# Optimization experiments

Measured on AMD Instinct MI355X. Metric: run time of the kernel, lower is better.

The kernel has to match this reference:

```python
import jax, jax.numpy as jnp
import numpy as np

N_NODES = 50000
N_EDGES = 640000
DIM_IN = 128
DIM_OUT = 128
NUM_GRAPHS = 64


def setup_inputs() -> dict:
    key = jax.random.key(0)
    ks = jax.random.split(key, 8)
    x = jax.random.normal(ks[0], (N_NODES, DIM_IN), dtype=jnp.float32)
    edge_index = jax.random.randint(ks[1], (2, N_EDGES), 0, N_NODES, dtype=jnp.int32)
    batch = jnp.sort(jax.random.randint(ks[2], (N_NODES,), 0, NUM_GRAPHS, dtype=jnp.int32))
    s = 1.0 / np.sqrt(DIM_IN)
    W1 = jax.random.normal(ks[3], (DIM_IN, DIM_IN), dtype=jnp.float32) * s
    W2 = jax.random.normal(ks[4], (DIM_IN, DIM_IN), dtype=jnp.float32) * s
    Wlin = jax.random.normal(ks[5], (DIM_IN, DIM_OUT), dtype=jnp.float32) * s
    b1 = jnp.zeros((DIM_IN,), jnp.float32)
    b2 = jnp.zeros((DIM_IN,), jnp.float32)
    blin = jnp.zeros((DIM_OUT,), jnp.float32)
    return {"x": x, "edge_index": edge_index, "batch": batch,
            "W1": W1, "b1": b1, "W2": W2, "b2": b2, "Wlin": Wlin, "blin": blin}


def _gcn_conv(x, W, b, src, dst, n_nodes):
    # GCNConv: symmetric norm with self-loops: D^{-1/2}(A+I)D^{-1/2} X W + b
    h = x @ W                                                   # [N, d]
    deg = jax.ops.segment_sum(jnp.ones_like(dst, jnp.float32), dst,
                              num_segments=n_nodes) + 1.0       # +1 self loop
    dinv = jax.lax.rsqrt(deg)                                   # [N]
    w = dinv[src] * dinv[dst]                                   # per-edge norm [E]
    agg = jax.ops.segment_sum(h[src] * w[:, None], dst, num_segments=n_nodes)
    return agg + h * (dinv * dinv)[:, None] + b                 # self-loop term + bias


def reference(x, edge_index, batch, W1, b1, W2, b2, Wlin, blin):
    n = x.shape[0]
    src, dst = edge_index[0], edge_index[1]
    h = jax.nn.relu(_gcn_conv(x, W1, b1, src, dst, n))          # dropout = identity (eval)
    h = _gcn_conv(h, W2, b2, src, dst, n)
    # global mean pool over graphs
    s = jax.ops.segment_sum(h, batch, num_segments=NUM_GRAPHS)  # [G, d]
    cnt = jax.ops.segment_sum(jnp.ones((n,), jnp.float32), batch, num_segments=NUM_GRAPHS)
    pooled = s / jnp.maximum(cnt, 1.0)[:, None]
    return jax.nn.relu(pooled @ Wlin + blin)
```

## Files before the change

### kernel.cpp

```cpp
#include <hip/hip_runtime.h>

#define N_NODES   50000
#define N_EDGES   640000
#define DIM       128
#define NUM_GRAPHS 64
#define SLOTS     64
#define FILL_BLOCKS  1250
#define GEMM1_BLOCKS 196

typedef __attribute__((ext_vector_type(8))) short          s16x8;
typedef __attribute__((ext_vector_type(8))) unsigned short u16x8;
typedef __attribute__((ext_vector_type(4))) float          f32x4;

__device__ inline float bf2f(unsigned short u) {
    unsigned v = ((unsigned)u) << 16;
    float f;
    __builtin_memcpy(&f, &v, 4);
    return f;
}
__device__ inline unsigned short f2bf(float f) {
    unsigned u;
    __builtin_memcpy(&u, &f, 4);
    u = (u + 0x7fffu + ((u >> 16) & 1u)) >> 16;
    return (unsigned short)u;
}

__global__ __launch_bounds__(128) void k_prep_w(const float* __restrict__ W1,
                                                const float* __restrict__ W2,
                                                unsigned short* __restrict__ Wt1,
                                                unsigned short* __restrict__ Wt2,
                                                int* __restrict__ cnt,
                                                float* __restrict__ pooled) {
    int k = blockIdx.x & 127;
    const float*    W  = (blockIdx.x < DIM) ? W1 : W2;
    unsigned short* Wt = (blockIdx.x < DIM) ? Wt1 : Wt2;
    int n = threadIdx.x;
    Wt[n * DIM + k] = f2bf(W[k * DIM + n]);

    int gid = blockIdx.x * 128 + threadIdx.x;
    for (int i = gid; i < N_NODES; i += 32768) cnt[i] = 0;
    if (gid < NUM_GRAPHS * DIM) pooled[gid] = 0.f;
}

__global__ __launch_bounds__(512) void k_fill_gemm1(const int* __restrict__ src,
                                                    const int* __restrict__ dst,
                                                    int* __restrict__ cnt,
                                                    unsigned short* __restrict__ slots,
                                                    const float* __restrict__ x,
                                                    const unsigned short* __restrict__ Wt1,
                                                    unsigned short* __restrict__ H1) {
    __shared__ unsigned short wsh[DIM][136];
    const int tid = threadIdx.x;

    if (blockIdx.x < FILL_BLOCKS) {
        int e = blockIdx.x * 512 + tid;
        int s = src[e], d = dst[e];
        int p = atomicAdd(&cnt[d], 1);
        if (p < SLOTS) slots[d * SLOTS + p] = (unsigned short)s;
        return;
    }

    const int gb = blockIdx.x - FILL_BLOCKS;

    #pragma unroll
    for (int i = 0; i < 4; i++) {
        int off = tid * 8 + i * 4096;
        int r = off >> 7, cc = off & 127;
        u16x8 v = *reinterpret_cast<const u16x8*>(Wt1 + off);
        *reinterpret_cast<u16x8*>(&wsh[r][cc]) = v;
    }
    __syncthreads();

    const int wid  = tid >> 6;
    const int lane = tid & 63;
    const int l15  = lane & 15;
    const int lk   = lane >> 4;
    const int row0 = gb * 256 + wid * 32;

    f32x4 acc[2][8];
    #pragma unroll
    for (int a = 0; a < 2; a++)
        #pragma unroll
        for (int n = 0; n < 8; n++) acc[a][n] = (f32x4){0.f, 0.f, 0.f, 0.f};

    const long long r0 = min(row0 + l15,      N_NODES - 1);
    const long long r1 = min(row0 + 16 + l15, N_NODES - 1);

    #pragma unroll
    for (int kk = 0; kk < 4; kk++) {
        const int kb = kk * 32 + lk * 8;
        s16x8 a0, a1;
        const float4 p0 = *reinterpret_cast<const float4*>(x + r0 * DIM + kb);
        const float4 q0 = *reinterpret_cast<const float4*>(x + r0 * DIM + kb + 4);
        const float4 p1 = *reinterpret_cast<const float4*>(x + r1 * DIM + kb);
        const float4 q1 = *reinterpret_cast<const float4*>(x + r1 * DIM + kb + 4);
        a0[0]=(short)f2bf(p0.x); a0[1]=(short)f2bf(p0.y); a0[2]=(short)f2bf(p0.z); a0[3]=(short)f2bf(p0.w);
        a0[4]=(short)f2bf(q0.x); a0[5]=(short)f2bf(q0.y); a0[6]=(short)f2bf(q0.z); a0[7]=(short)f2bf(q0.w);
        a1[0]=(short)f2bf(p1.x); a1[1]=(short)f2bf(p1.y); a1[2]=(short)f2bf(p1.z); a1[3]=(short)f2bf(p1.w);
        a1[4]=(short)f2bf(q1.x); a1[5]=(short)f2bf(q1.y); a1[6]=(short)f2bf(q1.z); a1[7]=(short)f2bf(q1.w);
        #pragma unroll
        for (int n = 0; n < 8; n++) {
            s16x8 b = *reinterpret_cast<const s16x8*>(&wsh[n * 16 + l15][kb]);
            acc[0][n] = __builtin_amdgcn_mfma_f32_16x16x32_bf16(a0, b, acc[0][n], 0, 0, 0);
            acc[1][n] = __builtin_amdgcn_mfma_f32_16x16x32_bf16(a1, b, acc[1][n], 0, 0, 0);
        }
    }

    #pragma unroll
    for (int rh = 0; rh < 2; rh++) {
        #pragma unroll
        for (int j = 0; j < 4; j++) {
            int row = row0 + rh * 16 + lk * 4 + j;
            if (row < N_NODES) {
                #pragma unroll
                for (int n = 0; n < 8; n++)
                    H1[(long long)row * DIM + n * 16 + l15] = f2bf(acc[rh][n][j]);
            }
        }
    }
}

__global__ __launch_bounds__(512) void k_gemm2(const unsigned short* __restrict__ Ab,
                                               const unsigned short* __restrict__ Wt,
                                               unsigned short* __restrict__ H) {
    __shared__ unsigned short wsh[DIM][136];
    const int tid = threadIdx.x;

    #pragma unroll
    for (int i = 0; i < 4; i++) {
        int off = tid * 8 + i * 4096;
        int r = off >> 7, cc = off & 127;
        u16x8 v = *reinterpret_cast<const u16x8*>(Wt + off);
        *reinterpret_cast<u16x8*>(&wsh[r][cc]) = v;
    }
    __syncthreads();

    const int wid  = tid >> 6;
    const int lane = tid & 63;
    const int l15  = lane & 15;
    const int lk   = lane >> 4;
    const int row0 = blockIdx.x * 256 + wid * 32;

    f32x4 acc[2][8];
    #pragma unroll
    for (int a = 0; a < 2; a++)
        #pragma unroll
        for (int n = 0; n < 8; n++) acc[a][n] = (f32x4){0.f, 0.f, 0.f, 0.f};

    const long long r0 = min(row0 + l15,      N_NODES - 1);
    const long long r1 = min(row0 + 16 + l15, N_NODES - 1);

    #pragma unroll
    for (int kk = 0; kk < 4; kk++) {
        const int kb = kk * 32 + lk * 8;
        s16x8 a0 = *reinterpret_cast<const s16x8*>(Ab + r0 * DIM + kb);
        s16x8 a1 = *reinterpret_cast<const s16x8*>(Ab + r1 * DIM + kb);
        #pragma unroll
        for (int n = 0; n < 8; n++) {
            s16x8 b = *reinterpret_cast<const s16x8*>(&wsh[n * 16 + l15][kb]);
            acc[0][n] = __builtin_amdgcn_mfma_f32_16x16x32_bf16(a0, b, acc[0][n], 0, 0, 0);
            acc[1][n] = __builtin_amdgcn_mfma_f32_16x16x32_bf16(a1, b, acc[1][n], 0, 0, 0);
        }
    }

    #pragma unroll
    for (int rh = 0; rh < 2; rh++) {
        #pragma unroll
        for (int j = 0; j < 4; j++) {
            int row = row0 + rh * 16 + lk * 4 + j;
            if (row < N_NODES) {
                #pragma unroll
                for (int n = 0; n < 8; n++)
                    H[(long long)row * DIM + n * 16 + l15] = f2bf(acc[rh][n][j]);
            }
        }
    }
}

__device__ inline void gather_node(const int* __restrict__ cnt,
                                   const unsigned short* __restrict__ slots,
                                   const unsigned short* __restrict__ h,
                                   const float* __restrict__ bias,
                                   int n, int c, float dn, float* acc) {
    float d2 = dn * dn;
    u16x8 hv = *reinterpret_cast<const u16x8*>(h + (size_t)n * DIM + c);
    #pragma unroll
    for (int j = 0; j < 8; j++) acc[j] = bf2f(hv[j]) * d2 + bias[c + j];

    const int m = min(cnt[n], SLOTS);
    const unsigned short* sl = slots + (size_t)n * SLOTS;

    int i = 0;
    for (; i + 3 < m; i += 4) {
        int s0 = sl[i], s1 = sl[i + 1], s2 = sl[i + 2], s3 = sl[i + 3];
        float w0 = rsqrtf((float)cnt[s0] + 1.0f) * dn;
        float w1 = rsqrtf((float)cnt[s1] + 1.0f) * dn;
        float w2 = rsqrtf((float)cnt[s2] + 1.0f) * dn;
        float w3 = rsqrtf((float)cnt[s3] + 1.0f) * dn;
        u16x8 v0 = *reinterpret_cast<const u16x8*>(h + (size_t)s0 * DIM + c);
        u16x8 v1 = *reinterpret_cast<const u16x8*>(h + (size_t)s1 * DIM + c);
        u16x8 v2 = *reinterpret_cast<const u16x8*>(h + (size_t)s2 * DIM + c);
        u16x8 v3 = *reinterpret_cast<const u16x8*>(h + (size_t)s3 * DIM + c);
        #pragma unroll
        for (int j = 0; j < 8; j++)
            acc[j] += (bf2f(v0[j]) * w0 + bf2f(v1[j]) * w1) +
                      (bf2f(v2[j]) * w2 + bf2f(v3[j]) * w3);
    }
    for (; i < m; i++) {
        int s0 = sl[i];
        float w0 = rsqrtf((float)cnt[s0] + 1.0f) * dn;
        u16x8 v0 = *reinterpret_cast<const u16x8*>(h + (size_t)s0 * DIM + c);
        #pragma unroll
        for (int j = 0; j < 8; j++) acc[j] += bf2f(v0[j]) * w0;
    }
}

__global__ __launch_bounds__(256) void k_pull1(const int* __restrict__ cnt,
                                               const unsigned short* __restrict__ slots,
                                               const unsigned short* __restrict__ h,
                                               const float* __restrict__ bias,
                                               unsigned short* __restrict__ outp) {
    int gid = blockIdx.x * blockDim.x + threadIdx.x;
    int n = gid >> 4;
    if (n >= N_NODES) return;
    int c = (gid & 15) << 3;

    float dn = rsqrtf((float)cnt[n] + 1.0f);
    float acc[8];
    gather_node(cnt, slots, h, bias, n, c, dn, acc);

    u16x8 o;
    #pragma unroll
    for (int j = 0; j < 8; j++) o[j] = f2bf(fmaxf(acc[j], 0.f));
    *reinterpret_cast<u16x8*>(outp + (size_t)n * DIM + c) = o;
}

__global__ __launch_bounds__(256) void k_pull_pool(const int* __restrict__ cnt,
                                                   const unsigned short* __restrict__ slots,
                                                   const unsigned short* __restrict__ h,
                                                   const float* __restrict__ bias,
                                                   const int* __restrict__ batch,
                                                   float* __restrict__ pooled) {
    __shared__ float pool_l[2][DIM];
    const int tid  = threadIdx.x;
    const int base = blockIdx.x * 64;
    const int c    = (tid & 15) << 3;

    pool_l[tid >> 7][tid & 127] = 0.f;
    __syncthreads();

    const int gmin = batch[min(base, N_NODES - 1)];

    #pragma unroll
    for (int r = 0; r < 4; r++) {
        int n = base + r * 16 + (tid >> 4);
        bool valid = n < N_NODES;
        int nn = min(n, N_NODES - 1);

        float dn = rsqrtf((float)cnt[nn] + 1.0f);
        float acc[8];
        gather_node(cnt, slots, h, bias, nn, c, dn, acc);
        if (!valid) {
            #pragma unroll
            for (int j = 0; j < 8; j++) acc[j] = 0.f;
        }

        const int g = batch[nn];
        const int d = g - gmin;

        if (__all(g == __shfl(g, 0))) {
            #pragma unroll
            for (int j = 0; j < 8; j++) {
                acc[j] += __shfl_xor(acc[j], 16);
                acc[j] += __shfl_xor(acc[j], 32);
            }
            if ((tid & 63) < 16) {
                if (d < 2) {
                    #pragma unroll
                    for (int j = 0; j < 8; j++) atomicAdd(&pool_l[d][c + j], acc[j]);
                } else {
                    #pragma unroll
                    for (int j = 0; j < 8; j++) atomicAdd(&pooled[g * DIM + c + j], acc[j]);
                }
            }
        } else {
            if (d < 2) {
                #pragma unroll
                for (int j = 0; j < 8; j++) atomicAdd(&pool_l[d][c + j], acc[j]);
            } else {
                #pragma unroll
                for (int j = 0; j < 8; j++) atomicAdd(&pooled[g * DIM + c + j], acc[j]);
            }
        }
    }
    __syncthreads();

    const int f = tid & 127;
    if (tid < 128) {
        atomicAdd(&pooled[gmin * DIM + f], pool_l[0][f]);
    } else {
        int last = min(base + 63, N_NODES - 1);
        if (batch[last] > gmin) atomicAdd(&pooled[(gmin + 1) * DIM + f], pool_l[1][f]);
    }
}

__global__ __launch_bounds__(128) void k_pool2(const float* __restrict__ pooled,
                                               const int* __restrict__ batch,
                                               const float* __restrict__ Wlin,
                                               const float* __restrict__ blin,
                                               float* __restrict__ out) {
    int g = blockIdx.x;
    int t = threadIdx.x;
    __shared__ int se[2];
    __shared__ float pr[DIM];
    if (t < 2) {
        int target = g + t;
        int lo = 0, hi = N_NODES;
        while (lo < hi) { int mid = (lo + hi) >> 1; if (batch[mid] < target) lo = mid + 1; else hi = mid; }
        se[t] = lo;
    }
    __syncthreads();
    float inv_cnt = 1.0f / fmaxf((float)(se[1] - se[0]), 1.0f);
    pr[t] = pooled[g * DIM + t] * inv_cnt;
    __syncthreads();
    float acc = blin[t];
    #pragma unroll 8
    for (int k = 0; k < DIM; k++) acc += pr[k] * Wlin[k * DIM + t];
    out[g * DIM + t] = fmaxf(acc, 0.f);
}

extern "C" void kernel_launch(void* const* d_in, const int* in_sizes, int n_in,
                              void* d_out, int out_size, void* d_ws, size_t ws_size,
                              hipStream_t stream) {
    const float* x          = (const float*)d_in[0];
    const int*   edge_index = (const int*)d_in[1];
    const int*   batch      = (const int*)d_in[2];
    const float* W1         = (const float*)d_in[3];
    const float* b1         = (const float*)d_in[4];
    const float* W2         = (const float*)d_in[5];
    const float* b2         = (const float*)d_in[6];
    const float* Wlin       = (const float*)d_in[7];
    const float* blin       = (const float*)d_in[8];
    float*       out        = (float*)d_out;

    const int* src = edge_index;
    const int* dst = edge_index + N_EDGES;

    char* ws = (char*)d_ws;
    size_t off = 0;
    auto alloc = [&](size_t bytes) { void* p = ws + off; off = (off + bytes + 255) & ~255ULL; return p; };
    int*            cnt    = (int*)            alloc((size_t)N_NODES * 4);
    unsigned short* slots  = (unsigned short*) alloc((size_t)N_NODES * SLOTS * 2);
    float*          pooled = (float*)          alloc((size_t)NUM_GRAPHS * DIM * 4);
    unsigned short* Wt1    = (unsigned short*) alloc((size_t)DIM * DIM * 2);
    unsigned short* Wt2    = (unsigned short*) alloc((size_t)DIM * DIM * 2);
    unsigned short* H1     = (unsigned short*) alloc((size_t)N_NODES * DIM * 2);
    unsigned short* Z1     = (unsigned short*) alloc((size_t)N_NODES * DIM * 2);
    unsigned short* H2     = (unsigned short*) alloc((size_t)N_NODES * DIM * 2);

    const int pull1Blocks = (N_NODES * 16 + 255) / 256;
    const int poolBlocks  = (N_NODES + 63) / 64;
    const int gemmBlocks  = (N_NODES + 255) / 256;

    k_prep_w<<<2 * DIM, DIM, 0, stream>>>(W1, W2, Wt1, Wt2, cnt, pooled);

    k_fill_gemm1<<<FILL_BLOCKS + GEMM1_BLOCKS, 512, 0, stream>>>(src, dst, cnt, slots, x, Wt1, H1);

    k_pull1<<<pull1Blocks, 256, 0, stream>>>(cnt, slots, H1, b1, Z1);

    k_gemm2<<<gemmBlocks, 512, 0, stream>>>(Z1, Wt2, H2);

    k_pull_pool<<<poolBlocks, 256, 0, stream>>>(cnt, slots, H2, b2, batch, pooled);

    k_pool2<<<NUM_GRAPHS, 128, 0, stream>>>(pooled, batch, Wlin, blin, out);
}
```

Before: 133.9 us.

## Partition edge fill by destination range to localize atomics and slot writes

The edge-fill part of the fused fill/GEMM1 kernel is restructured. Each of 320 fill blocks now scans a 16000-edge slice with vectorized int4 loads and handles only edges whose destination falls in one of eight node ranges. The intent is to keep atomic counter updates and slot writes within a smaller, more cache-local region. The cost is that each edge is read eight times, and block order changes so the GEMM blocks launch first.

```diff
diff --git a/kernel.cpp b/kernel.cpp
--- a/kernel.cpp
+++ b/kernel.cpp
@@ -5,8 +5,10 @@
 #define DIM       128
 #define NUM_GRAPHS 64
 #define SLOTS     64
-#define FILL_BLOCKS  1250
 #define GEMM1_BLOCKS 196
+#define FILL_BLOCKS  320
+#define NODES_PER_BUCKET 6250
+#define EDGES_PER_SLICE  16000
 
 typedef __attribute__((ext_vector_type(8))) short          s16x8;
 typedef __attribute__((ext_vector_type(8))) unsigned short u16x8;
@@ -52,15 +54,37 @@
     __shared__ unsigned short wsh[DIM][136];
     const int tid = threadIdx.x;
 
-    if (blockIdx.x < FILL_BLOCKS) {
-        int e = blockIdx.x * 512 + tid;
-        int s = src[e], d = dst[e];
-        int p = atomicAdd(&cnt[d], 1);
-        if (p < SLOTS) slots[d * SLOTS + p] = (unsigned short)s;
+    if (blockIdx.x >= GEMM1_BLOCKS) {
+        const int fb    = blockIdx.x - GEMM1_BLOCKS;
+        const int range = blockIdx.x & 7;
+        const int rb    = fb >> 3;
+        const int lo    = range * NODES_PER_BUCKET;
+        const int hi    = lo + NODES_PER_BUCKET;
+        const int ebase = rb * EDGES_PER_SLICE;
+
+        for (int g = tid; g < EDGES_PER_SLICE / 4; g += 512) {
+            int e = ebase + g * 4;
+            int4 s4 = *reinterpret_cast<const int4*>(src + e);
+            int4 d4 = *reinterpret_cast<const int4*>(dst + e);
+            if (d4.x >= lo && d4.x < hi) {
+                int p = atomicAdd(&cnt[d4.x], 1);
+                if (p < SLOTS) slots[d4.x * SLOTS + p] = (unsigned short)s4.x;
+            }
+            if (d4.y >= lo && d4.y < hi) {
+                int p = atomicAdd(&cnt[d4.y], 1);
+                if (p < SLOTS) slots[d4.y * SLOTS + p] = (unsigned short)s4.y;
+            }
+            if (d4.z >= lo && d4.z < hi) {
+                int p = atomicAdd(&cnt[d4.z], 1);
+                if (p < SLOTS) slots[d4.z * SLOTS + p] = (unsigned short)s4.z;
+            }
+            if (d4.w >= lo && d4.w < hi) {
+                int p = atomicAdd(&cnt[d4.w], 1);
+                if (p < SLOTS) slots[d4.w * SLOTS + p] = (unsigned short)s4.w;
+            }
+        }
         return;
     }
-
-    const int gb = blockIdx.x - FILL_BLOCKS;
 
     #pragma unroll
     for (int i = 0; i < 4; i++) {
@@ -75,7 +99,7 @@
     const int lane = tid & 63;
     const int l15  = lane & 15;
     const int lk   = lane >> 4;
-    const int row0 = gb * 256 + wid * 32;
+    const int row0 = blockIdx.x * 256 + wid * 32;
 
     f32x4 acc[2][8];
     #pragma unroll
@@ -364,7 +388,7 @@
 
     k_prep_w<<<2 * DIM, DIM, 0, stream>>>(W1, W2, Wt1, Wt2, cnt, pooled);
 
-    k_fill_gemm1<<<FILL_BLOCKS + GEMM1_BLOCKS, 512, 0, stream>>>(src, dst, cnt, slots, x, Wt1, H1);
+    k_fill_gemm1<<<GEMM1_BLOCKS + FILL_BLOCKS, 512, 0, stream>>>(src, dst, cnt, slots, x, Wt1, H1);
 
     k_pull1<<<pull1Blocks, 256, 0, stream>>>(cnt, slots, H1, b1, Z1);
 
```

Result: faster. 126.6 us (-5.5%).
